# Kernel optimization log

Hardware: AMD Instinct MI355X
Metric: run time of the kernel (lower is better)

Reference implementation:

```python
import jax, jax.numpy as jnp
import numpy as np

B, T, H, NH = 2, 2048, 1024, 16
HD = H // NH


def setup_inputs() -> dict:
    key = jax.random.key(0)
    ks = jax.random.split(key, 12)
    s = 1.0 / np.sqrt(H)
    inp = {
        "q": jax.random.normal(ks[0], (B, T, H), jnp.float32),
        "k": jax.random.normal(ks[1], (B, T, H), jnp.float32),
        "v": jax.random.normal(ks[2], (B, T, H), jnp.float32),
        "mask": jnp.tril(jnp.ones((T, T), jnp.int32))[None, None],  # causal [1,1,T,T]
        "w_q": jax.random.normal(ks[3], (H, H), jnp.float32) * s,
        "b_q": jax.random.normal(ks[4], (H,), jnp.float32) * 0.01,
        "w_k": jax.random.normal(ks[5], (H, H), jnp.float32) * s,
        "b_k": jax.random.normal(ks[6], (H,), jnp.float32) * 0.01,
        "w_v": jax.random.normal(ks[7], (H, H), jnp.float32) * s,
        "b_v": jax.random.normal(ks[8], (H,), jnp.float32) * 0.01,
        "w_o": jax.random.normal(ks[9], (H, H), jnp.float32) * s,
        "b_o": jax.random.normal(ks[10], (H,), jnp.float32) * 0.01,
    }
    return inp


def reference(q, k, v, mask, w_q, b_q, w_k, b_k, w_v, b_v, w_o, b_o):
    def split_heads(x):
        Bx, Tx, _ = x.shape
        return x.reshape(Bx, Tx, NH, HD).transpose(0, 2, 1, 3)  # [B,NH,T,HD]

    Q = split_heads(q @ w_q.T + b_q)
    K = split_heads(k @ w_k.T + b_k)
    V = split_heads(v @ w_v.T + b_v)

    scores = jnp.einsum("bhqd,bhkd->bhqk", Q, K) / np.sqrt(HD).astype(np.float32)
    scores = jnp.where(mask == 0, jnp.float32(-1e9), scores)
    weights = jax.nn.softmax(scores, axis=-1)  # dropout prob = 0.0
    out = jnp.einsum("bhqk,bhkd->bhqd", weights, V)
    out = out.transpose(0, 2, 1, 3).reshape(q.shape[0], q.shape[1], H)
    return out @ w_o.T + b_o
```

## Files before the change

### kernel.cpp

```cpp
#include <hip/hip_runtime.h>
#include <hip/hip_bf16.h>

#define Bb 2
#define Tt 2048
#define Hh 1024
#define NHh 16

typedef short bf16x8 __attribute__((ext_vector_type(8)));
typedef float f32x4 __attribute__((ext_vector_type(4)));
typedef unsigned short u16;
typedef unsigned int u32;
typedef u16 u16x4v __attribute__((ext_vector_type(4)));
typedef u32 u32x2v __attribute__((ext_vector_type(2)));

#define QK_SCALE 0.180336880f

#if __has_builtin(__builtin_amdgcn_exp2f)
__device__ __forceinline__ float exp2_fast(float x) { return __builtin_amdgcn_exp2f(x); }
#else
__device__ __forceinline__ float exp2_fast(float x) { return __expf(x * 0.69314718f); }
#endif

__device__ __forceinline__ u16 f2b(float x) {
  unsigned u = __builtin_bit_cast(unsigned, x);
  u += 0x7FFFu + ((u >> 16) & 1u);
  return (u16)(u >> 16);
}
__device__ __forceinline__ float b2f(u16 x) {
  return __builtin_bit_cast(float, (u32)x << 16);
}

__device__ __forceinline__ u32 cvt_pk(float lo, float hi) {
  u32 r;
  asm("v_cvt_pk_bf16_f32 %0, %1, %2" : "=v"(r) : "v"(lo), "v"(hi));
  return r;
}

__global__ __launch_bounds__(256) void cvt_all_kernel(
    const float* __restrict__ q, const float* __restrict__ k, const float* __restrict__ v,
    const float* __restrict__ wq, const float* __restrict__ wk,
    const float* __restrict__ wv, const float* __restrict__ wo,
    u16* __restrict__ qb, u16* __restrict__ kb, u16* __restrict__ vb,
    u16* __restrict__ wqb, u16* __restrict__ wkb, u16* __restrict__ wvb,
    u16* __restrict__ wob, int n4_in, int n4_w) {
  const int which = blockIdx.y;
  const float* src;
  u16* dst;
  int n4;
  float sc = 1.0f;
  switch (which) {
    case 0: src = q;  dst = qb;  n4 = n4_in; break;
    case 1: src = k;  dst = kb;  n4 = n4_in; break;
    case 2: src = v;  dst = vb;  n4 = n4_in; break;
    case 3: src = wq; dst = wqb; n4 = n4_w; sc = QK_SCALE; break;
    case 4: src = wk; dst = wkb; n4 = n4_w; break;
    case 5: src = wv; dst = wvb; n4 = n4_w; break;
    default: src = wo; dst = wob; n4 = n4_w; break;
  }
  int i = blockIdx.x * blockDim.x + threadIdx.x;
  int stride = gridDim.x * blockDim.x;
  for (; i < n4; i += stride) {
    float4 vv = ((const float4*)src)[i];
    u16x4v o;
    o.x = f2b(vv.x * sc); o.y = f2b(vv.y * sc); o.z = f2b(vv.z * sc); o.w = f2b(vv.w * sc);
    ((u16x4v*)dst)[i] = o;
  }
}

template<int NF, int MODE>
__device__ __forceinline__ void gemm_body(const u16* __restrict__ A,
                                          const u16* __restrict__ W,
                                          const float* __restrict__ bias, float bscale,
                                          void* __restrict__ Cout,
                                          u16* lA, u16* lB, int mt, int nt) {
  const int tid = threadIdx.x;
  const int lane = tid & 63;
  const int wid = tid >> 6;
  const int wr = wid >> 1, wc = wid & 1;
  const int g = lane >> 4, fr = lane & 15;
  constexpr int NT = NF * 32;

  f32x4 acc[4][NF];
#pragma unroll
  for (int m = 0; m < 4; ++m)
#pragma unroll
    for (int n = 0; n < NF; ++n) acc[m][n] = (f32x4){0.f, 0.f, 0.f, 0.f};

  const int srow = tid >> 3;
  const int scol = (tid & 7) * 8;

  bf16x8 ra[4], rb[NF];
#pragma unroll
  for (int ps = 0; ps < 4; ++ps)
    ra[ps] = *(const bf16x8*)(A + (size_t)(mt * 128 + ps * 32 + srow) * Hh + scol);
#pragma unroll
  for (int ps = 0; ps < NF; ++ps)
    rb[ps] = *(const bf16x8*)(W + (size_t)(nt * NT + ps * 32 + srow) * Hh + scol);
#pragma unroll
  for (int ps = 0; ps < 4; ++ps) {
    int r = ps * 32 + srow;
    *(bf16x8*)((char*)lA + r * 128 + ((scol * 2) ^ ((r & 7) << 4))) = ra[ps];
  }
#pragma unroll
  for (int ps = 0; ps < NF; ++ps) {
    int r = ps * 32 + srow;
    *(bf16x8*)((char*)lB + r * 128 + ((scol * 2) ^ ((r & 7) << 4))) = rb[ps];
  }
  __syncthreads();

  for (int kt = 0; kt < Hh; kt += 64) {
    if (kt + 64 < Hh) {
#pragma unroll
      for (int ps = 0; ps < 4; ++ps)
        ra[ps] = *(const bf16x8*)(A + (size_t)(mt * 128 + ps * 32 + srow) * Hh + kt + 64 + scol);
#pragma unroll
      for (int ps = 0; ps < NF; ++ps)
        rb[ps] = *(const bf16x8*)(W + (size_t)(nt * NT + ps * 32 + srow) * Hh + kt + 64 + scol);
    }
    bf16x8 af[4][2], bfv[NF][2];
#pragma unroll
    for (int m = 0; m < 4; ++m)
#pragma unroll
      for (int ks = 0; ks < 2; ++ks) {
        int r = wr * 64 + m * 16 + fr;
        af[m][ks] = *(const bf16x8*)((const char*)lA + r * 128 + ((ks * 64 + g * 16) ^ ((r & 7) << 4)));
      }
#pragma unroll
    for (int n = 0; n < NF; ++n)
#pragma unroll
      for (int ks = 0; ks < 2; ++ks) {
        int r = wc * (NT / 2) + n * 16 + fr;
        bfv[n][ks] = *(const bf16x8*)((const char*)lB + r * 128 + ((ks * 64 + g * 16) ^ ((r & 7) << 4)));
      }
#pragma unroll
    for (int m = 0; m < 4; ++m)
#pragma unroll
      for (int n = 0; n < NF; ++n)
#pragma unroll
        for (int ks = 0; ks < 2; ++ks)
          acc[m][n] = __builtin_amdgcn_mfma_f32_16x16x32_bf16(af[m][ks], bfv[n][ks],
                                                              acc[m][n], 0, 0, 0);
    if (kt + 64 < Hh) {
      __syncthreads();
#pragma unroll
      for (int ps = 0; ps < 4; ++ps) {
        int r = ps * 32 + srow;
        *(bf16x8*)((char*)lA + r * 128 + ((scol * 2) ^ ((r & 7) << 4))) = ra[ps];
      }
#pragma unroll
      for (int ps = 0; ps < NF; ++ps) {
        int r = ps * 32 + srow;
        *(bf16x8*)((char*)lB + r * 128 + ((scol * 2) ^ ((r & 7) << 4))) = rb[ps];
      }
      __syncthreads();
    }
  }

#pragma unroll
  for (int n = 0; n < NF; ++n) {
    int Cc = nt * NT + wc * (NT / 2) + n * 16 + fr;
    float bv = bias[Cc] * bscale;
#pragma unroll
    for (int m = 0; m < 4; ++m) {
#pragma unroll
      for (int j = 0; j < 4; ++j) {
        int R = mt * 128 + wr * 64 + m * 16 + g * 4 + j;
        float val = acc[m][n][j] + bv;
        if constexpr (MODE == 0) {
          int bb = R >> 11, t = R & (Tt - 1);
          int h = Cc >> 6, d = Cc & 63;
          ((u16*)Cout)[(((size_t)(bb * NHh + h) * Tt + t) << 6) + d] = f2b(val);
        } else if constexpr (MODE == 2) {
          int bb = R >> 11, t = R & (Tt - 1);
          int h = Cc >> 6, d = Cc & 63;
          ((u16*)Cout)[(((size_t)(bb * NHh + h) * 64 + d) << 11) + t] = f2b(val);
        } else {
          ((float*)Cout)[(size_t)R * Hh + Cc] = val;
        }
      }
    }
  }
}

__global__ __launch_bounds__(256, 3) void proj_qkv_kernel(
    const u16* __restrict__ qb, const u16* __restrict__ kb, const u16* __restrict__ vb,
    const u16* __restrict__ wqb, const u16* __restrict__ wkb, const u16* __restrict__ wvb,
    const float* __restrict__ biq, const float* __restrict__ bik, const float* __restrict__ biv,
    u16* __restrict__ Qp, u16* __restrict__ Kp, u16* __restrict__ Vt) {
  __shared__ u16 lA[128 * 64];
  __shared__ u16 lB[128 * 64];
  const int id = blockIdx.x;
  const int nt = (id >> 3) & 7;
  const int slot = (id & 7) + 8 * (id >> 6);
  const int z = slot >> 5, mt = slot & 31;
  if (z == 0)      gemm_body<4, 0>(qb, wqb, biq, QK_SCALE, Qp, lA, lB, mt, nt);
  else if (z == 1) gemm_body<4, 0>(kb, wkb, bik, 1.0f, Kp, lA, lB, mt, nt);
  else             gemm_body<4, 2>(vb, wvb, biv, 1.0f, Vt, lA, lB, mt, nt);
}

__global__ __launch_bounds__(256, 2) void gemm_out_kernel(
    const u16* __restrict__ A, const u16* __restrict__ W,
    const float* __restrict__ bias, float* __restrict__ Cout) {
  __shared__ u16 lA[128 * 64];
  __shared__ u16 lB[64 * 64];
  const int id = blockIdx.x;
  const int j = id >> 3;
  const int mt = (id & 7) + 8 * (j >> 4);
  const int nt = j & 15;
  gemm_body<2, 1>(A, W, bias, 1.0f, Cout, lA, lB, mt, nt);
}

__global__ __launch_bounds__(512, 6) void attn_kernel(const u16* __restrict__ Qp,
                                                      const u16* __restrict__ Kp,
                                                      const u16* __restrict__ Vt,
                                                      u16* __restrict__ AO,
                                                      u16* __restrict__ Obuf,
                                                      float2* __restrict__ MLbuf) {
  __shared__ u16 lK[2][64 * 64];
  __shared__ u16 lV[2][64 * 64];
  __shared__ u16 lP[128 * 64];
  const int tid = threadIdx.x;
  const int lane = tid & 63;
  const int w = tid >> 6;
  const int g = lane >> 4, fr = lane & 15;

  const int id = blockIdx.x;
  const int bh_lo = id & 7;
  const int j = id >> 3;
  const int kk = j >> 5;
  const int grp = (j >> 3) & 3;
  const int s = j & 7;
  const int bh = grp * 8 + bh_lo;
  int qt, kv0, kv1, chunk = 0;
  bool split;
  if (kk == 0) { qt = 8 + s; kv0 = 0; kv1 = 15; split = true; }
  else if (kk == 1) {
    if ((s & 1) == 0) { qt = 7 - (s >> 1); kv0 = 0; kv1 = 2 * qt + 1; split = false; }
    else { qt = 15 - (s >> 1); kv0 = 16; kv1 = 2 * qt + 1; split = true; chunk = 1; }
  } else {
    if ((s & 1) == 0) { qt = (s >> 1); kv0 = 0; kv1 = 2 * qt + 1; split = false; }
    else { qt = 8 + (s >> 1); kv0 = 16; kv1 = 2 * qt + 1; split = true; chunk = 1; }
  }
  const int q0 = qt * 128;

  bf16x8 qf[2];
  {
    const u16* qrow = Qp + (((size_t)bh * Tt + q0 + w * 16 + fr) << 6) + g * 8;
    qf[0] = *(const bf16x8*)(qrow);
    qf[1] = *(const bf16x8*)(qrow + 32);
  }

  const int srow = tid >> 3;
  const int scol = (tid & 7) * 8;
  const int sswz = (scol * 2) ^ ((srow & 7) << 4);

  bf16x8 rk, rv;
  rk = *(const bf16x8*)(Kp + (((size_t)bh * Tt + kv0 * 64 + srow) << 6) + scol);
  rv = *(const bf16x8*)(Vt + (((size_t)bh * 64 + srow) << 11) + kv0 * 64 + scol);
  *(bf16x8*)((char*)lK[0] + srow * 128 + sswz) = rk;
  *(bf16x8*)((char*)lV[0] + srow * 128 + sswz) = rv;
  __syncthreads();

  float m_r = -1e30f, l_r = 0.f;
  f32x4 acc[4];
#pragma unroll
  for (int nd = 0; nd < 4; ++nd) acc[nd] = (f32x4){0.f, 0.f, 0.f, 0.f};

  const int prow = w * 16 + fr;
  const int psw = (prow & 7) << 4;
  const int qrow = w * 16 + fr;

  for (int jt = kv0; jt <= kv1; ++jt) {
    const char* bK = (const char*)lK[jt & 1];
    const char* bV = (const char*)lV[jt & 1];
    if (jt < kv1) {
      rk = *(const bf16x8*)(Kp + (((size_t)bh * Tt + (jt + 1) * 64 + srow) << 6) + scol);
      rv = *(const bf16x8*)(Vt + (((size_t)bh * 64 + srow) << 11) + (jt + 1) * 64 + scol);
    }
    f32x4 sv4[4];
    __builtin_amdgcn_s_setprio(1);
#pragma unroll
    for (int n = 0; n < 4; ++n) {
      sv4[n] = (f32x4){0.f, 0.f, 0.f, 0.f};
      int rbase = (n * 16 + fr) * 128;
      int rsw = (fr & 7) << 4;
#pragma unroll
      for (int ks = 0; ks < 2; ++ks) {
        bf16x8 ak = *(const bf16x8*)(bK + rbase + ((ks * 64 + g * 16) ^ rsw));
        sv4[n] = __builtin_amdgcn_mfma_f32_16x16x32_bf16(ak, qf[ks], sv4[n], 0, 0, 0);
      }
    }
    __builtin_amdgcn_s_setprio(0);

    float tm = -1e30f;
    if (jt >= 2 * qt) {
      const int dj = (jt - 2 * qt) << 6;
#pragma unroll
      for (int n = 0; n < 4; ++n)
#pragma unroll
        for (int r = 0; r < 4; ++r) {
          if (dj + n * 16 + g * 4 + r > qrow) sv4[n][r] = -1e30f;
          tm = fmaxf(tm, sv4[n][r]);
        }
    } else {
#pragma unroll
      for (int n = 0; n < 4; ++n)
#pragma unroll
        for (int r = 0; r < 4; ++r) tm = fmaxf(tm, sv4[n][r]);
    }
    tm = fmaxf(tm, __shfl_xor(tm, 16));
    tm = fmaxf(tm, __shfl_xor(tm, 32));
    if (!__all(tm <= m_r + 8.0f)) {
      float mn = fmaxf(m_r, tm);
      float sc = exp2_fast(m_r - mn);
      m_r = mn;
      l_r *= sc;
      float scj[4];
#pragma unroll
      for (int j2 = 0; j2 < 4; ++j2) scj[j2] = __shfl(sc, g * 4 + j2);
#pragma unroll
      for (int nd = 0; nd < 4; ++nd)
#pragma unroll
        for (int j2 = 0; j2 < 4; ++j2) acc[nd][j2] *= scj[j2];
    }
    float rs = 0.f;
    u32 pw[4][2];
#pragma unroll
    for (int n = 0; n < 4; ++n) {
      float p0 = exp2_fast(sv4[n][0] - m_r);
      float p1 = exp2_fast(sv4[n][1] - m_r);
      float p2 = exp2_fast(sv4[n][2] - m_r);
      float p3 = exp2_fast(sv4[n][3] - m_r);
      rs += (p0 + p1) + (p2 + p3);
      pw[n][0] = cvt_pk(p0, p1);
      pw[n][1] = cvt_pk(p2, p3);
    }
    rs += __shfl_xor(rs, 16);
    rs += __shfl_xor(rs, 32);
    l_r += rs;
    bf16x8 pa[2];
    {
      char* base = (char*)lP + prow * 128;
#pragma unroll
      for (int n = 0; n < 4; ++n)
        *(u32x2v*)(base + ((32 * n + 8 * g) ^ psw)) = (u32x2v){pw[n][0], pw[n][1]};
#pragma unroll
      for (int ks = 0; ks < 2; ++ks)
        pa[ks] = *(const bf16x8*)(base + ((ks * 64 + g * 16) ^ psw));
    }
    __builtin_amdgcn_s_setprio(1);
#pragma unroll
    for (int nd = 0; nd < 4; ++nd) {
      int rbase = (nd * 16 + fr) * 128;
      int rsw = (fr & 7) << 4;
#pragma unroll
      for (int ks = 0; ks < 2; ++ks) {
        bf16x8 bv = *(const bf16x8*)(bV + rbase + ((ks * 64 + g * 16) ^ rsw));
        acc[nd] = __builtin_amdgcn_mfma_f32_16x16x32_bf16(pa[ks], bv, acc[nd], 0, 0, 0);
      }
    }
    __builtin_amdgcn_s_setprio(0);
    if (jt < kv1) {
      *(bf16x8*)((char*)lK[(jt + 1) & 1] + srow * 128 + sswz) = rk;
      *(bf16x8*)((char*)lV[(jt + 1) & 1] + srow * 128 + sswz) = rv;
      __syncthreads();
    }
  }

  if (!split) {
    const int b = bh >> 4, hh = bh & 15;
    float lj[4];
#pragma unroll
    for (int j2 = 0; j2 < 4; ++j2) lj[j2] = __shfl(l_r, g * 4 + j2);
#pragma unroll
    for (int j2 = 0; j2 < 4; ++j2) {
      float inv = 1.0f / lj[j2];
      int qq = q0 + w * 16 + g * 4 + j2;
      size_t base = (((size_t)b * Tt + qq) << 10) + hh * 64;
#pragma unroll
      for (int nd = 0; nd < 4; ++nd)
        AO[base + nd * 16 + fr] = f2b(acc[nd][j2] * inv);
    }
  } else {
    const int pidx = ((bh * 8 + (qt - 8)) << 1) + chunk;
    if (g == 0) MLbuf[pidx * 128 + w * 16 + fr] = make_float2(m_r, l_r);
    u16* ob = Obuf + (size_t)pidx * 8192;
#pragma unroll
    for (int j2 = 0; j2 < 4; ++j2) {
      int row = w * 16 + g * 4 + j2;
#pragma unroll
      for (int nd = 0; nd < 4; ++nd)
        ob[row * 64 + nd * 16 + fr] = f2b(acc[nd][j2]);
    }
  }
}

__global__ __launch_bounds__(256) void merge_kernel(const u16* __restrict__ Obuf,
                                                    const float2* __restrict__ MLbuf,
                                                    u16* __restrict__ AO) {
  const int row_id = blockIdx.x * 256 + threadIdx.x;
  const int bh = row_id >> 10;
  const int qs = (row_id >> 7) & 7;
  const int row = row_id & 127;
  const int tile = bh * 8 + qs;
  float2 ml0 = MLbuf[(tile * 2 + 0) * 128 + row];
  float2 ml1 = MLbuf[(tile * 2 + 1) * 128 + row];
  float M = fmaxf(ml0.x, ml1.x);
  float w0 = exp2_fast(ml0.x - M);
  float w1 = exp2_fast(ml1.x - M);
  float inv = 1.0f / (w0 * ml0.y + w1 * ml1.y);
  const u16* o0 = Obuf + (size_t)(tile * 2 + 0) * 8192 + row * 64;
  const u16* o1 = Obuf + (size_t)(tile * 2 + 1) * 8192 + row * 64;
  const int qt = 8 + qs;
  const int qq = qt * 128 + row;
  const int b = bh >> 4, hh = bh & 15;
  u16* dst = AO + (((size_t)b * Tt + qq) << 10) + hh * 64;
#pragma unroll
  for (int c = 0; c < 8; ++c) {
    bf16x8 v0 = *(const bf16x8*)(o0 + c * 8);
    bf16x8 v1 = *(const bf16x8*)(o1 + c * 8);
    bf16x8 o;
#pragma unroll
    for (int e = 0; e < 8; ++e)
      o[e] = (short)f2b((w0 * b2f((u16)v0[e]) + w1 * b2f((u16)v1[e])) * inv);
    *(bf16x8*)(dst + c * 8) = o;
  }
}

extern "C" void kernel_launch(void* const* d_in, const int* in_sizes, int n_in,
                              void* d_out, int out_size, void* d_ws, size_t ws_size,
                              hipStream_t stream) {
  const float* q   = (const float*)d_in[0];
  const float* k   = (const float*)d_in[1];
  const float* v   = (const float*)d_in[2];
  const float* wq  = (const float*)d_in[4];
  const float* bq  = (const float*)d_in[5];
  const float* wk  = (const float*)d_in[6];
  const float* bk  = (const float*)d_in[7];
  const float* wv  = (const float*)d_in[8];
  const float* bv  = (const float*)d_in[9];
  const float* wo  = (const float*)d_in[10];
  const float* bo  = (const float*)d_in[11];

  char* ws = (char*)d_ws;
  const size_t SZB = (size_t)Bb * Tt * Hh * 2;
  const size_t WB  = (size_t)Hh * Hh * 2;
  u16* qb  = (u16*)(ws);
  u16* kb  = (u16*)(ws + SZB);
  u16* vb  = (u16*)(ws + 2 * SZB);
  u16* wqb = (u16*)(ws + 3 * SZB);
  u16* wkb = (u16*)(ws + 3 * SZB + WB);
  u16* wvb = (u16*)(ws + 3 * SZB + 2 * WB);
  u16* wob = (u16*)(ws + 3 * SZB + 3 * WB);
  u16* Qp  = (u16*)(ws + 3 * SZB + 4 * WB);
  u16* Kp  = (u16*)(ws + 4 * SZB + 4 * WB);
  u16* Vt  = (u16*)(ws + 5 * SZB + 4 * WB);
  u16* AO  = qb;
  u16* Obuf = kb;
  float2* MLbuf = (float2*)vb;

  const int N4_IN = (Bb * Tt * Hh) / 4;
  const int N4_W  = (Hh * Hh) / 4;
  cvt_all_kernel<<<dim3(512, 7), 256, 0, stream>>>(
      q, k, v, wq, wk, wv, wo, qb, kb, vb, wqb, wkb, wvb, wob, N4_IN, N4_W);

  proj_qkv_kernel<<<dim3(768), 256, 0, stream>>>(
      qb, kb, vb, wqb, wkb, wvb, bq, bk, bv, Qp, Kp, Vt);

  attn_kernel<<<dim3(768), 512, 0, stream>>>(Qp, Kp, Vt, AO, Obuf, MLbuf);

  merge_kernel<<<dim3(128), 256, 0, stream>>>(Obuf, MLbuf, AO);

  gemm_out_kernel<<<dim3(512), 256, 0, stream>>>(
      AO, wob, bo, (float*)d_out);
}
```

Measured before the change: 120.6 us.

## Process two 16-row query slices per wave in attention with 256-thread blocks

```diff
diff --git a/kernel.cpp b/kernel.cpp
--- a/kernel.cpp
+++ b/kernel.cpp
@@ -210,7 +210,7 @@
   gemm_body<2, 1>(A, W, bias, 1.0f, Cout, lA, lB, mt, nt);
 }
 
-__global__ __launch_bounds__(512, 6) void attn_kernel(const u16* __restrict__ Qp,
+__global__ __launch_bounds__(256, 4) void attn_kernel(const u16* __restrict__ Qp,
                                                       const u16* __restrict__ Kp,
                                                       const u16* __restrict__ Vt,
                                                       u16* __restrict__ AO,
@@ -218,7 +218,7 @@
                                                       float2* __restrict__ MLbuf) {
   __shared__ u16 lK[2][64 * 64];
   __shared__ u16 lV[2][64 * 64];
-  __shared__ u16 lP[128 * 64];
+  __shared__ u16 lP[64 * 64];
   const int tid = threadIdx.x;
   const int lane = tid & 63;
   const int w = tid >> 6;
@@ -243,110 +243,130 @@
   }
   const int q0 = qt * 128;
 
-  bf16x8 qf[2];
-  {
-    const u16* qrow = Qp + (((size_t)bh * Tt + q0 + w * 16 + fr) << 6) + g * 8;
-    qf[0] = *(const bf16x8*)(qrow);
-    qf[1] = *(const bf16x8*)(qrow + 32);
+  bf16x8 qf[2][2];
+#pragma unroll
+  for (int h = 0; h < 2; ++h) {
+    const u16* qrow = Qp + (((size_t)bh * Tt + q0 + w * 32 + h * 16 + fr) << 6) + g * 8;
+    qf[h][0] = *(const bf16x8*)(qrow);
+    qf[h][1] = *(const bf16x8*)(qrow + 32);
   }
 
   const int srow = tid >> 3;
   const int scol = (tid & 7) * 8;
   const int sswz = (scol * 2) ^ ((srow & 7) << 4);
 
-  bf16x8 rk, rv;
-  rk = *(const bf16x8*)(Kp + (((size_t)bh * Tt + kv0 * 64 + srow) << 6) + scol);
-  rv = *(const bf16x8*)(Vt + (((size_t)bh * 64 + srow) << 11) + kv0 * 64 + scol);
-  *(bf16x8*)((char*)lK[0] + srow * 128 + sswz) = rk;
-  *(bf16x8*)((char*)lV[0] + srow * 128 + sswz) = rv;
+  bf16x8 rk[2], rv[2];
+#pragma unroll
+  for (int ps = 0; ps < 2; ++ps) {
+    rk[ps] = *(const bf16x8*)(Kp + (((size_t)bh * Tt + kv0 * 64 + ps * 32 + srow) << 6) + scol);
+    rv[ps] = *(const bf16x8*)(Vt + (((size_t)bh * 64 + ps * 32 + srow) << 11) + kv0 * 64 + scol);
+  }
+#pragma unroll
+  for (int ps = 0; ps < 2; ++ps) {
+    *(bf16x8*)((char*)lK[0] + (ps * 32 + srow) * 128 + sswz) = rk[ps];
+    *(bf16x8*)((char*)lV[0] + (ps * 32 + srow) * 128 + sswz) = rv[ps];
+  }
   __syncthreads();
 
-  float m_r = -1e30f, l_r = 0.f;
-  f32x4 acc[4];
-#pragma unroll
-  for (int nd = 0; nd < 4; ++nd) acc[nd] = (f32x4){0.f, 0.f, 0.f, 0.f};
+  float m_r[2] = {-1e30f, -1e30f}, l_r[2] = {0.f, 0.f};
+  f32x4 acc[2][4];
+#pragma unroll
+  for (int h = 0; h < 2; ++h)
+#pragma unroll
+    for (int nd = 0; nd < 4; ++nd) acc[h][nd] = (f32x4){0.f, 0.f, 0.f, 0.f};
 
   const int prow = w * 16 + fr;
   const int psw = (prow & 7) << 4;
-  const int qrow = w * 16 + fr;
 
   for (int jt = kv0; jt <= kv1; ++jt) {
     const char* bK = (const char*)lK[jt & 1];
     const char* bV = (const char*)lV[jt & 1];
     if (jt < kv1) {
-      rk = *(const bf16x8*)(Kp + (((size_t)bh * Tt + (jt + 1) * 64 + srow) << 6) + scol);
-      rv = *(const bf16x8*)(Vt + (((size_t)bh * 64 + srow) << 11) + (jt + 1) * 64 + scol);
-    }
-    f32x4 sv4[4];
+#pragma unroll
+      for (int ps = 0; ps < 2; ++ps) {
+        rk[ps] = *(const bf16x8*)(Kp + (((size_t)bh * Tt + (jt + 1) * 64 + ps * 32 + srow) << 6) + scol);
+        rv[ps] = *(const bf16x8*)(Vt + (((size_t)bh * 64 + ps * 32 + srow) << 11) + (jt + 1) * 64 + scol);
+      }
+    }
+    f32x4 sv[2][4];
+#pragma unroll
+    for (int h = 0; h < 2; ++h)
+#pragma unroll
+      for (int n = 0; n < 4; ++n) sv[h][n] = (f32x4){0.f, 0.f, 0.f, 0.f};
     __builtin_amdgcn_s_setprio(1);
 #pragma unroll
     for (int n = 0; n < 4; ++n) {
-      sv4[n] = (f32x4){0.f, 0.f, 0.f, 0.f};
       int rbase = (n * 16 + fr) * 128;
       int rsw = (fr & 7) << 4;
 #pragma unroll
       for (int ks = 0; ks < 2; ++ks) {
         bf16x8 ak = *(const bf16x8*)(bK + rbase + ((ks * 64 + g * 16) ^ rsw));
-        sv4[n] = __builtin_amdgcn_mfma_f32_16x16x32_bf16(ak, qf[ks], sv4[n], 0, 0, 0);
+        sv[0][n] = __builtin_amdgcn_mfma_f32_16x16x32_bf16(ak, qf[0][ks], sv[0][n], 0, 0, 0);
+        sv[1][n] = __builtin_amdgcn_mfma_f32_16x16x32_bf16(ak, qf[1][ks], sv[1][n], 0, 0, 0);
       }
     }
     __builtin_amdgcn_s_setprio(0);
 
-    float tm = -1e30f;
-    if (jt >= 2 * qt) {
-      const int dj = (jt - 2 * qt) << 6;
-#pragma unroll
-      for (int n = 0; n < 4; ++n)
-#pragma unroll
-        for (int r = 0; r < 4; ++r) {
-          if (dj + n * 16 + g * 4 + r > qrow) sv4[n][r] = -1e30f;
-          tm = fmaxf(tm, sv4[n][r]);
-        }
-    } else {
-#pragma unroll
-      for (int n = 0; n < 4; ++n)
-#pragma unroll
-        for (int r = 0; r < 4; ++r) tm = fmaxf(tm, sv4[n][r]);
-    }
-    tm = fmaxf(tm, __shfl_xor(tm, 16));
-    tm = fmaxf(tm, __shfl_xor(tm, 32));
-    if (!__all(tm <= m_r + 8.0f)) {
-      float mn = fmaxf(m_r, tm);
-      float sc = exp2_fast(m_r - mn);
-      m_r = mn;
-      l_r *= sc;
-      float scj[4];
-#pragma unroll
-      for (int j2 = 0; j2 < 4; ++j2) scj[j2] = __shfl(sc, g * 4 + j2);
-#pragma unroll
-      for (int nd = 0; nd < 4; ++nd)
-#pragma unroll
-        for (int j2 = 0; j2 < 4; ++j2) acc[nd][j2] *= scj[j2];
-    }
-    float rs = 0.f;
-    u32 pw[4][2];
-#pragma unroll
-    for (int n = 0; n < 4; ++n) {
-      float p0 = exp2_fast(sv4[n][0] - m_r);
-      float p1 = exp2_fast(sv4[n][1] - m_r);
-      float p2 = exp2_fast(sv4[n][2] - m_r);
-      float p3 = exp2_fast(sv4[n][3] - m_r);
-      rs += (p0 + p1) + (p2 + p3);
-      pw[n][0] = cvt_pk(p0, p1);
-      pw[n][1] = cvt_pk(p2, p3);
-    }
-    rs += __shfl_xor(rs, 16);
-    rs += __shfl_xor(rs, 32);
-    l_r += rs;
-    bf16x8 pa[2];
-    {
-      char* base = (char*)lP + prow * 128;
-#pragma unroll
-      for (int n = 0; n < 4; ++n)
-        *(u32x2v*)(base + ((32 * n + 8 * g) ^ psw)) = (u32x2v){pw[n][0], pw[n][1]};
-#pragma unroll
-      for (int ks = 0; ks < 2; ++ks)
-        pa[ks] = *(const bf16x8*)(base + ((ks * 64 + g * 16) ^ psw));
+    const bool needmask = (jt >= 2 * qt);
+    const int dj = needmask ? ((jt - 2 * qt) << 6) : 0;
+    bf16x8 pa[2][2];
+#pragma unroll
+    for (int h = 0; h < 2; ++h) {
+      const int qrw = w * 32 + h * 16 + fr;
+      float tm = -1e30f;
+      if (needmask) {
+#pragma unroll
+        for (int n = 0; n < 4; ++n)
+#pragma unroll
+          for (int r = 0; r < 4; ++r) {
+            if (dj + n * 16 + g * 4 + r > qrw) sv[h][n][r] = -1e30f;
+            tm = fmaxf(tm, sv[h][n][r]);
+          }
+      } else {
+#pragma unroll
+        for (int n = 0; n < 4; ++n)
+#pragma unroll
+          for (int r = 0; r < 4; ++r) tm = fmaxf(tm, sv[h][n][r]);
+      }
+      tm = fmaxf(tm, __shfl_xor(tm, 16));
+      tm = fmaxf(tm, __shfl_xor(tm, 32));
+      if (!__all(tm <= m_r[h] + 8.0f)) {
+        float mn = fmaxf(m_r[h], tm);
+        float sc = exp2_fast(m_r[h] - mn);
+        m_r[h] = mn;
+        l_r[h] *= sc;
+        float scj[4];
+#pragma unroll
+        for (int j2 = 0; j2 < 4; ++j2) scj[j2] = __shfl(sc, g * 4 + j2);
+#pragma unroll
+        for (int nd = 0; nd < 4; ++nd)
+#pragma unroll
+          for (int j2 = 0; j2 < 4; ++j2) acc[h][nd][j2] *= scj[j2];
+      }
+      float rs = 0.f;
+      u32 pw[4][2];
+#pragma unroll
+      for (int n = 0; n < 4; ++n) {
+        float p0 = exp2_fast(sv[h][n][0] - m_r[h]);
+        float p1 = exp2_fast(sv[h][n][1] - m_r[h]);
+        float p2 = exp2_fast(sv[h][n][2] - m_r[h]);
+        float p3 = exp2_fast(sv[h][n][3] - m_r[h]);
+        rs += (p0 + p1) + (p2 + p3);
+        pw[n][0] = cvt_pk(p0, p1);
+        pw[n][1] = cvt_pk(p2, p3);
+      }
+      rs += __shfl_xor(rs, 16);
+      rs += __shfl_xor(rs, 32);
+      l_r[h] += rs;
+      {
+        char* base = (char*)lP + prow * 128;
+#pragma unroll
+        for (int n = 0; n < 4; ++n)
+          *(u32x2v*)(base + ((32 * n + 8 * g) ^ psw)) = (u32x2v){pw[n][0], pw[n][1]};
+#pragma unroll
+        for (int ks = 0; ks < 2; ++ks)
+          pa[h][ks] = *(const bf16x8*)(base + ((ks * 64 + g * 16) ^ psw));
+      }
     }
     __builtin_amdgcn_s_setprio(1);
 #pragma unroll
@@ -356,41 +376,51 @@
 #pragma unroll
       for (int ks = 0; ks < 2; ++ks) {
         bf16x8 bv = *(const bf16x8*)(bV + rbase + ((ks * 64 + g * 16) ^ rsw));
-        acc[nd] = __builtin_amdgcn_mfma_f32_16x16x32_bf16(pa[ks], bv, acc[nd], 0, 0, 0);
+        acc[0][nd] = __builtin_amdgcn_mfma_f32_16x16x32_bf16(pa[0][ks], bv, acc[0][nd], 0, 0, 0);
+        acc[1][nd] = __builtin_amdgcn_mfma_f32_16x16x32_bf16(pa[1][ks], bv, acc[1][nd], 0, 0, 0);
       }
     }
     __builtin_amdgcn_s_setprio(0);
     if (jt < kv1) {
-      *(bf16x8*)((char*)lK[(jt + 1) & 1] + srow * 128 + sswz) = rk;
-      *(bf16x8*)((char*)lV[(jt + 1) & 1] + srow * 128 + sswz) = rv;
+#pragma unroll
+      for (int ps = 0; ps < 2; ++ps) {
+        *(bf16x8*)((char*)lK[(jt + 1) & 1] + (ps * 32 + srow) * 128 + sswz) = rk[ps];
+        *(bf16x8*)((char*)lV[(jt + 1) & 1] + (ps * 32 + srow) * 128 + sswz) = rv[ps];
+      }
       __syncthreads();
     }
   }
 
   if (!split) {
     const int b = bh >> 4, hh = bh & 15;
-    float lj[4];
-#pragma unroll
-    for (int j2 = 0; j2 < 4; ++j2) lj[j2] = __shfl(l_r, g * 4 + j2);
-#pragma unroll
-    for (int j2 = 0; j2 < 4; ++j2) {
-      float inv = 1.0f / lj[j2];
-      int qq = q0 + w * 16 + g * 4 + j2;
-      size_t base = (((size_t)b * Tt + qq) << 10) + hh * 64;
-#pragma unroll
-      for (int nd = 0; nd < 4; ++nd)
-        AO[base + nd * 16 + fr] = f2b(acc[nd][j2] * inv);
+#pragma unroll
+    for (int h = 0; h < 2; ++h) {
+      float lj[4];
+#pragma unroll
+      for (int j2 = 0; j2 < 4; ++j2) lj[j2] = __shfl(l_r[h], g * 4 + j2);
+#pragma unroll
+      for (int j2 = 0; j2 < 4; ++j2) {
+        float inv = 1.0f / lj[j2];
+        int qq = q0 + w * 32 + h * 16 + g * 4 + j2;
+        size_t base = (((size_t)b * Tt + qq) << 10) + hh * 64;
+#pragma unroll
+        for (int nd = 0; nd < 4; ++nd)
+          AO[base + nd * 16 + fr] = f2b(acc[h][nd][j2] * inv);
+      }
     }
   } else {
     const int pidx = ((bh * 8 + (qt - 8)) << 1) + chunk;
-    if (g == 0) MLbuf[pidx * 128 + w * 16 + fr] = make_float2(m_r, l_r);
-    u16* ob = Obuf + (size_t)pidx * 8192;
-#pragma unroll
-    for (int j2 = 0; j2 < 4; ++j2) {
-      int row = w * 16 + g * 4 + j2;
-#pragma unroll
-      for (int nd = 0; nd < 4; ++nd)
-        ob[row * 64 + nd * 16 + fr] = f2b(acc[nd][j2]);
+#pragma unroll
+    for (int h = 0; h < 2; ++h) {
+      if (g == 0) MLbuf[pidx * 128 + w * 32 + h * 16 + fr] = make_float2(m_r[h], l_r[h]);
+      u16* ob = Obuf + (size_t)pidx * 8192;
+#pragma unroll
+      for (int j2 = 0; j2 < 4; ++j2) {
+        int row = w * 32 + h * 16 + g * 4 + j2;
+#pragma unroll
+        for (int nd = 0; nd < 4; ++nd)
+          ob[row * 64 + nd * 16 + fr] = f2b(acc[h][nd][j2]);
+      }
     }
   }
 }
@@ -467,7 +497,7 @@
   proj_qkv_kernel<<<dim3(768), 256, 0, stream>>>(
       qb, kb, vb, wqb, wkb, wvb, bq, bk, bv, Qp, Kp, Vt);
 
-  attn_kernel<<<dim3(768), 512, 0, stream>>>(Qp, Kp, Vt, AO, Obuf, MLbuf);
+  attn_kernel<<<dim3(768), 256, 0, stream>>>(Qp, Kp, Vt, AO, Obuf, MLbuf);
 
   merge_kernel<<<dim3(128), 256, 0, stream>>>(Obuf, MLbuf, AO);
 
```

Result: slower. 148.8 us (+23.4%).
